# Optimization experiments

Hardware: AMD Instinct MI355X
Metric: run time of the kernel (lower is better)

## Reference

```python
import jax, jax.numpy as jnp
import numpy as np

TMP = 1.0          # concrete temperature (beta)
SAMPLE_BIAS = 0.0  # self.sample_bias

N_NODES = 10000
N_EDGES = 640000
D_EMB = 128
HIDDEN = 64


def setup_inputs() -> dict:
    key = jax.random.key(0)
    k_emb, k_ei, k_w1, k_w2 = jax.random.split(key, 4)
    embed = jax.random.normal(k_emb, (N_NODES, D_EMB), dtype=jnp.float32)
    edge_index = jax.random.randint(k_ei, (2, N_EDGES), 0, N_NODES, dtype=jnp.int64)
    W1 = jax.random.normal(k_w1, (2 * D_EMB, HIDDEN), dtype=jnp.float32) * 0.06
    b1 = jnp.zeros((HIDDEN,), dtype=jnp.float32)
    W2 = jax.random.normal(k_w2, (HIDDEN, 1), dtype=jnp.float32) * 0.12
    b2 = jnp.zeros((1,), dtype=jnp.float32)
    return {"embed": embed, "edge_index": edge_index, "W1": W1, "b1": b1, "W2": W2, "b2": b2}


def _concrete_sample(log_alpha, beta, key):
    # training=True branch: logistic noise through sigmoid gate
    u = jax.random.uniform(key, log_alpha.shape, dtype=log_alpha.dtype)
    u = u * (1.0 - 2.0 * SAMPLE_BIAS) + SAMPLE_BIAS
    noise = jnp.log(u) - jnp.log1p(-u)
    return jax.nn.sigmoid((noise + log_alpha) / beta)


def reference(embed, edge_index, W1, b1, W2, b2):
    N = embed.shape[0]
    col, row = edge_index[0], edge_index[1]
    # edge gather + concat: [E, 2*D]
    f12 = jnp.concatenate([embed[col], embed[row]], axis=-1)
    # tiny 2-layer MLP -> per-edge logit
    h = jax.nn.relu(f12 @ W1 + b1)
    log_alpha = (h @ W2 + b2).reshape(-1)  # [E]
    values = _concrete_sample(log_alpha, TMP, jax.random.key(42))
    # sparse_coo_tensor(...).to_dense() sums duplicate indices
    adj = jnp.zeros((N, N), dtype=embed.dtype).at[col, row].add(1.0)
    mask_dense = jnp.zeros((N, N), dtype=embed.dtype).at[col, row].add(values)
    sym_mask = (mask_dense + mask_dense.T) * 0.5
    masked_adj = adj * sym_mask
    return masked_adj
```

## Files before the change

kernel.cpp:

```cpp
#include <hip/hip_runtime.h>
#include <stdint.h>

#define D_EMB 128
#define HIDDEN 64
#define PACK_SCALE 1024.0f
#define INV_PACK (1.0f/1024.0f)
#define NODES_PER_BLK 8

__device__ __forceinline__ uint32_t rotl32(uint32_t x, int r) {
    return (x << r) | (x >> (32 - r));
}

__device__ __forceinline__ uint32_t jax_threefry_bits_part(uint32_t e) {
    const uint32_t ks0 = 0u;
    const uint32_t ks1 = 42u;
    const uint32_t ks2 = 0x1BD11BDAu ^ 0u ^ 42u;
    uint32_t x0 = 0u + ks0;
    uint32_t x1 = e + ks1;
#define TF_R(r) { x0 += x1; x1 = rotl32(x1, (r)); x1 ^= x0; }
    TF_R(13) TF_R(15) TF_R(26) TF_R(6)
    x0 += ks1; x1 += ks2 + 1u;
    TF_R(17) TF_R(29) TF_R(16) TF_R(24)
    x0 += ks2; x1 += ks0 + 2u;
    TF_R(13) TF_R(15) TF_R(26) TF_R(6)
    x0 += ks0; x1 += ks1 + 3u;
    TF_R(17) TF_R(29) TF_R(16) TF_R(24)
    x0 += ks1; x1 += ks2 + 4u;
    TF_R(13) TF_R(15) TF_R(26) TF_R(6)
    x0 += ks2; x1 += ks0 + 5u;
#undef TF_R
    return x0 ^ x1;
}

__device__ __forceinline__ float edge_gate_value(
    const float* __restrict__ Pcat, const float* __restrict__ w2s, float b2v,
    int c, int r, int e) {
    const float4* p1 = (const float4*)(Pcat + (size_t)c * (2 * HIDDEN));
    const float4* p2 = (const float4*)(Pcat + (size_t)r * (2 * HIDDEN) + HIDDEN);
    const float4* w4 = (const float4*)w2s;
    float la = b2v;
#pragma unroll
    for (int k = 0; k < HIDDEN / 4; k++) {
        float4 a = p1[k];
        float4 b = p2[k];
        float4 w = w4[k];
        la += fmaxf(a.x + b.x, 0.0f) * w.x + fmaxf(a.y + b.y, 0.0f) * w.y +
              fmaxf(a.z + b.z, 0.0f) * w.z + fmaxf(a.w + b.w, 0.0f) * w.w;
    }
    uint32_t bits = jax_threefry_bits_part((uint32_t)e);
    float u = __uint_as_float((bits >> 9) | 0x3f800000u) - 1.0f;
    return u / (u + (1.0f - u) * __expf(-la));
}

__global__ __launch_bounds__(256) void node_proj_kernel(
    const float* __restrict__ embed, const float* __restrict__ W1,
    const float* __restrict__ b1, float* __restrict__ Pcat, int N) {
    __shared__ float e_lds[NODES_PER_BLK][D_EMB];
    int n0 = blockIdx.x * NODES_PER_BLK;
    int t = threadIdx.x;
    {
        int node = n0 + (t >> 5);
        float4 v = make_float4(0.f, 0.f, 0.f, 0.f);
        if (node < N) v = ((const float4*)embed)[(size_t)n0 * (D_EMB / 4) + t];
        ((float4*)&e_lds[0][0])[t] = v;
    }
    __syncthreads();
#pragma unroll
    for (int rep = 0; rep < 4; rep++) {
        int idx = rep * 256 + t;
        int nl = idx >> 7;
        int col = idx & 127;
        int half = col >> 6, k = col & 63;
        const float* w = W1 + (size_t)half * D_EMB * HIDDEN + k;
        float acc = (half == 0) ? b1[k] : 0.0f;
        const float* ev = e_lds[nl];
#pragma unroll 16
        for (int d = 0; d < D_EMB; d++) acc += ev[d] * w[(size_t)d * HIDDEN];
        if (n0 + nl < N) Pcat[(size_t)(n0 + nl) * (2 * HIDDEN) + col] = acc;
    }
}

__global__ __launch_bounds__(256) void edge_scatter_kernel(
    const int* __restrict__ ei, const float* __restrict__ Pcat,
    const float* __restrict__ W2, const float* __restrict__ b2,
    float* __restrict__ out, int E, int N) {
    __shared__ float w2s[HIDDEN];
    if (threadIdx.x < HIDDEN) w2s[threadIdx.x] = W2[threadIdx.x];
    __syncthreads();
    int e = blockIdx.x * blockDim.x + threadIdx.x;
    if (e >= E) return;
    int c = ei[e];
    int r = ei[E + e];
    if ((unsigned)c >= (unsigned)N || (unsigned)r >= (unsigned)N) return;
    float v = edge_gate_value(Pcat, w2s, b2[0], c, r, e);
    atomicAdd(out + (size_t)c * N + r, PACK_SCALE + v);
}

__global__ __launch_bounds__(256) void edge_finalize_kernel(
    const int* __restrict__ ei, float* __restrict__ out, int E, int N) {
    int e = blockIdx.x * blockDim.x + threadIdx.x;
    if (e >= E) return;
    int c = ei[e];
    int r = ei[E + e];
    if ((unsigned)c >= (unsigned)N || (unsigned)r >= (unsigned)N) return;

    size_t own = (size_t)c * N + r;
    size_t mir = (size_t)r * N + c;
    float a = out[own];
    if (a < PACK_SCALE) return;
    float b = out[mir];
    if (c != r && b > 0.0f && b < PACK_SCALE) return;

    if (c <= r || b == 0.0f) {
        float cnt_a = truncf(a * INV_PACK);
        float s_a = a - PACK_SCALE * cnt_a;
        float cnt_b = truncf(b * INV_PACK);
        float s_b = b - PACK_SCALE * cnt_b;
        float sum = s_a + s_b;
        out[own] = cnt_a * 0.5f * sum;
        if (c < r && b != 0.0f) out[mir] = cnt_b * 0.5f * sum;
    }
}

extern "C" void kernel_launch(void* const* d_in, const int* in_sizes, int n_in,
                              void* d_out, int out_size, void* d_ws, size_t ws_size,
                              hipStream_t stream) {
    const float* embed = (const float*)d_in[0];
    const int*   ei    = (const int*)d_in[1];
    const float* W1    = (const float*)d_in[2];
    const float* b1    = (const float*)d_in[3];
    const float* W2    = (const float*)d_in[4];
    const float* b2    = (const float*)d_in[5];
    float* out = (float*)d_out;

    const int N = in_sizes[0] / D_EMB;
    const int E = in_sizes[1] / 2;

    float* Pcat = (float*)d_ws;

    hipMemsetAsync(d_out, 0, (size_t)out_size * sizeof(float), stream);

    node_proj_kernel<<<(N + NODES_PER_BLK - 1) / NODES_PER_BLK, 256, 0, stream>>>(
        embed, W1, b1, Pcat, N);

    const int eb = 256;
    const int eg = (E + eb - 1) / eb;
    edge_scatter_kernel<<<eg, eb, 0, stream>>>(ei, Pcat, W2, b2, out, E, N);
    edge_finalize_kernel<<<eg, eb, 0, stream>>>(ei, out, E, N);
}
```

Baseline: 219.5 us.

## Replace memset with nontemporal fill kernel and register-block node projection

The hipMemsetAsync of the dense N×N output is replaced by a custom kernel that zeroes memory with nontemporal 16-byte stores. The node projection now handles 32 nodes per block, and each thread keeps 16 accumulators so every W1 load is reused across 16 nodes instead of one. The aim is to cut the cost of the 400MB zero fill and the redundant weight traffic in the projection. The fill kernel does not cover the tail when out_size is not a multiple of 4, and the larger tile means fewer projection blocks.

```diff
diff --git a/kernel.cpp b/kernel.cpp
--- a/kernel.cpp
+++ b/kernel.cpp
@@ -5,7 +5,9 @@
 #define HIDDEN 64
 #define PACK_SCALE 1024.0f
 #define INV_PACK (1.0f/1024.0f)
-#define NODES_PER_BLK 8
+#define PN 32
+
+typedef __attribute__((ext_vector_type(4))) float f32x4;
 
 __device__ __forceinline__ uint32_t rotl32(uint32_t x, int r) {
     return (x << r) | (x >> (32 - r));
@@ -52,31 +54,53 @@
     return u / (u + (1.0f - u) * __expf(-la));
 }
 
+__global__ __launch_bounds__(256) void fill_zero_kernel(
+    f32x4* __restrict__ out, size_t n4) {
+    size_t base = ((size_t)blockIdx.x * 256 + threadIdx.x) * 4;
+    f32x4 z = {0.0f, 0.0f, 0.0f, 0.0f};
+#pragma unroll
+    for (int i = 0; i < 4; i++) {
+        size_t idx = base + i;
+        if (idx < n4) __builtin_nontemporal_store(z, &out[idx]);
+    }
+}
+
 __global__ __launch_bounds__(256) void node_proj_kernel(
     const float* __restrict__ embed, const float* __restrict__ W1,
     const float* __restrict__ b1, float* __restrict__ Pcat, int N) {
-    __shared__ float e_lds[NODES_PER_BLK][D_EMB];
-    int n0 = blockIdx.x * NODES_PER_BLK;
+    __shared__ float e_lds[PN][D_EMB];
+    int n0 = blockIdx.x * PN;
     int t = threadIdx.x;
     {
-        int node = n0 + (t >> 5);
-        float4 v = make_float4(0.f, 0.f, 0.f, 0.f);
-        if (node < N) v = ((const float4*)embed)[(size_t)n0 * (D_EMB / 4) + t];
-        ((float4*)&e_lds[0][0])[t] = v;
+        const float4* src = (const float4*)embed + (size_t)n0 * (D_EMB / 4);
+        float4* dst = (float4*)&e_lds[0][0];
+        for (int i = t; i < PN * (D_EMB / 4); i += 256) {
+            int node = n0 + (i >> 5);
+            float4 v = make_float4(0.f, 0.f, 0.f, 0.f);
+            if (node < N) v = src[i];
+            dst[i] = v;
+        }
     }
     __syncthreads();
+    int col = t & 127;
+    int nset = t >> 7;
+    int half = col >> 6, k = col & 63;
+    const float* w = W1 + (size_t)half * D_EMB * HIDDEN + k;
+    float bias = (half == 0) ? b1[k] : 0.0f;
+    float acc[16];
 #pragma unroll
-    for (int rep = 0; rep < 4; rep++) {
-        int idx = rep * 256 + t;
-        int nl = idx >> 7;
-        int col = idx & 127;
-        int half = col >> 6, k = col & 63;
-        const float* w = W1 + (size_t)half * D_EMB * HIDDEN + k;
-        float acc = (half == 0) ? b1[k] : 0.0f;
-        const float* ev = e_lds[nl];
-#pragma unroll 16
-        for (int d = 0; d < D_EMB; d++) acc += ev[d] * w[(size_t)d * HIDDEN];
-        if (n0 + nl < N) Pcat[(size_t)(n0 + nl) * (2 * HIDDEN) + col] = acc;
+    for (int j = 0; j < 16; j++) acc[j] = bias;
+    const int nb = nset * 16;
+#pragma unroll 8
+    for (int d = 0; d < D_EMB; d++) {
+        float wd = w[(size_t)d * HIDDEN];
+#pragma unroll
+        for (int j = 0; j < 16; j++) acc[j] += e_lds[nb + j][d] * wd;
+    }
+#pragma unroll
+    for (int j = 0; j < 16; j++) {
+        int node = n0 + nb + j;
+        if (node < N) Pcat[(size_t)node * (2 * HIDDEN) + col] = acc[j];
     }
 }
 
@@ -138,10 +162,11 @@
 
     float* Pcat = (float*)d_ws;
 
-    hipMemsetAsync(d_out, 0, (size_t)out_size * sizeof(float), stream);
+    size_t n4 = (size_t)out_size / 4;
+    size_t fill_blocks = (n4 + 1023) / 1024;
+    fill_zero_kernel<<<(uint32_t)fill_blocks, 256, 0, stream>>>((f32x4*)out, n4);
 
-    node_proj_kernel<<<(N + NODES_PER_BLK - 1) / NODES_PER_BLK, 256, 0, stream>>>(
-        embed, W1, b1, Pcat, N);
+    node_proj_kernel<<<(N + PN - 1) / PN, 256, 0, stream>>>(embed, W1, b1, Pcat, N);
 
     const int eb = 256;
     const int eg = (E + eb - 1) / eb;
```

Result: slower. 636.6 us (+190.0%).
